# Performance work log

Hardware: AMD Instinct MI355X
Metric: run time of the kernel (lower is better)

The kernel has to match this reference:

```python
import jax, jax.numpy as jnp
import numpy as np

B, T, D = 2, 1024, 1024
NUM_HEADS_ARG = 16
HS = D // NUM_HEADS_ARG          # 64 (per-head size)
H = HS                           # bug in source: num_heads passed = head_size -> 64 heads
FF = 4 * D
EPS = 1e-5


def _layernorm(x, gamma, beta):
    mu = jnp.mean(x, axis=-1, keepdims=True)
    var = jnp.mean(jnp.square(x - mu), axis=-1, keepdims=True)
    return (x - mu) * jax.lax.rsqrt(var + EPS) * gamma + beta


def setup_inputs() -> dict:
    key = jax.random.key(0)
    ks = jax.random.split(key, 12)
    s_d = 1.0 / np.sqrt(D)
    s_cat = 1.0 / np.sqrt(H * HS)
    s_ff = 1.0 / np.sqrt(FF)
    return {
        "x": jax.random.normal(ks[0], (B, T, D), jnp.float32),
        "Wq": jax.random.uniform(ks[1], (H, D, HS), jnp.float32, -s_d, s_d),
        "Wk": jax.random.uniform(ks[2], (H, D, HS), jnp.float32, -s_d, s_d),
        "Wv": jax.random.uniform(ks[3], (H, D, HS), jnp.float32, -s_d, s_d),
        "Wo": jax.random.uniform(ks[4], (H * HS, D), jnp.float32, -s_cat, s_cat),
        "bo": jax.random.uniform(ks[5], (D,), jnp.float32, -s_cat, s_cat),
        "W1": jax.random.uniform(ks[6], (D, FF), jnp.float32, -s_d, s_d),
        "b1": jax.random.uniform(ks[7], (FF,), jnp.float32, -s_d, s_d),
        "W2": jax.random.uniform(ks[8], (FF, D), jnp.float32, -s_ff, s_ff),
        "b2": jax.random.uniform(ks[9], (D,), jnp.float32, -s_ff, s_ff),
        "g1": jnp.ones((D,), jnp.float32),
        "be1": jnp.zeros((D,), jnp.float32),
        "g2": jnp.ones((D,), jnp.float32),
        "be2": jnp.zeros((D,), jnp.float32),
    }


def reference(x, Wq, Wk, Wv, Wo, bo, W1, b1, W2, b2, g1, be1, g2, be2):
    # per-head projections (no bias): [B,H,T,hs]
    q = jnp.einsum('btd,hde->bhte', x, Wq)
    k = jnp.einsum('btd,hde->bhte', x, Wk)
    v = jnp.einsum('btd,hde->bhte', x, Wv)
    scores = jnp.einsum('bhte,bhse->bhts', q, k) / np.sqrt(HS)  # [B,H,T,T]
    causal = jnp.tril(jnp.ones((T, T), bool))
    scores = jnp.where(causal, scores, -jnp.inf)
    probs = jax.nn.softmax(scores, axis=-1)
    att = jnp.einsum('bhts,bhse->bhte', probs, v)               # [B,H,T,hs]
    # torch stack(dim=3) -> [B,T,hs,H] then flatten: index = d*H + h
    cat = jnp.transpose(att, (0, 2, 3, 1)).reshape(B, T, HS * H)
    mha = cat @ Wo + bo
    x1 = _layernorm(x + mha, g1, be1)
    ff = jax.nn.relu(x1 @ W1 + b1) @ W2 + b2
    return _layernorm(x1 + ff, g2, be2)
```

## Files before the change

kernel.cpp:

```cpp
#include <hip/hip_runtime.h>

typedef unsigned short u16;
typedef __bf16 bf16x8 __attribute__((ext_vector_type(8)));
typedef float f32x4 __attribute__((ext_vector_type(4)));

#define B_ 2
#define T_ 1024
#define D_ 1024
#define H_ 64
#define HS_ 64
#define FF_ 4096
#define SZ_QKV 8388608L
#define S_SCALE 0.1803368801111f

__device__ __forceinline__ float bf2f(u16 u) {
  union { unsigned int v; float f; } x; x.v = ((unsigned int)u) << 16; return x.f;
}
__device__ __forceinline__ u16 f2bf(float f) {
  union { float f; unsigned int v; } x; x.f = f;
  unsigned int r = x.v + 0x7fffu + ((x.v >> 16) & 1u);
  return (u16)(r >> 16);
}
__device__ __forceinline__ u16 f2bf_rtz(float f) {
  union { float f; unsigned int v; } x; x.f = f;
  return (u16)(x.v >> 16);
}

typedef __attribute__((address_space(3))) unsigned int lds_u32;
typedef __attribute__((address_space(1))) const unsigned int glb_u32;
__device__ __forceinline__ void gload_lds16(const void* g, void* l) {
  __builtin_amdgcn_global_load_lds((glb_u32*)g, (lds_u32*)l, 16, 0, 0);
}

__global__ __launch_bounds__(256) void prep(
    const float* __restrict__ x, const float* __restrict__ Wq,
    const float* __restrict__ Wk, const float* __restrict__ Wv,
    const float* __restrict__ Wo, const float* __restrict__ W1,
    const float* __restrict__ W2,
    u16* __restrict__ xb, u16* __restrict__ Wqkvt, u16* __restrict__ Wot,
    u16* __restrict__ W1t, u16* __restrict__ W2t)
{
  __shared__ float tile[64][65];
  int id = blockIdx.x;
  if (id < 1024) {
    const long i = ((long)id * 256 + threadIdx.x) * 8;
    float4 a = *(const float4*)(x + i);
    float4 b = *(const float4*)(x + i + 4);
    union { uint4 v; u16 u[8]; } o;
    o.u[0]=f2bf(a.x); o.u[1]=f2bf(a.y); o.u[2]=f2bf(a.z); o.u[3]=f2bf(a.w);
    o.u[4]=f2bf(b.x); o.u[5]=f2bf(b.y); o.u[6]=f2bf(b.z); o.u[7]=f2bf(b.w);
    *(uint4*)(xb + i) = o.v;
    return;
  }
  id -= 1024;
  const float* in; u16* out; long ibase, obase; int in_rs, out_rs, r0, c0;
  if (id < 3072) {
    const int w = id >> 10, rem = id & 1023;
    const int z = rem >> 4, rt = rem & 15;
    in = (w == 0) ? Wq : (w == 1) ? Wk : Wv;
    ibase = (long)z * 65536; in_rs = 64; r0 = rt * 64; c0 = 0;
    out = Wqkvt + (long)w * 4194304;
    obase = (long)z * 65536; out_rs = 1024;
  } else if (id < 4096) {
    const int rem = id - 3072;
    const int z = rem >> 4, ct = rem & 15;
    in = Wo; ibase = (long)z * 1024; in_rs = 65536; r0 = 0; c0 = ct * 64;
    out = Wot; obase = (long)z * 64; out_rs = 4096;
  } else if (id < 5120) {
    const int rem = id - 4096;
    const int rt = rem >> 6, ct = rem & 63;
    in = W1; ibase = 0; in_rs = 4096; r0 = rt * 64; c0 = ct * 64;
    out = W1t; obase = 0; out_rs = 1024;
  } else {
    const int rem = id - 5120;
    const int rt = rem >> 4, ct = rem & 15;
    in = W2; ibase = 0; in_rs = 1024; r0 = rt * 64; c0 = ct * 64;
    out = W2t; obase = 0; out_rs = 4096;
  }
  const int t = threadIdx.x, lr = t >> 4, lc4 = (t & 15) * 4;
  #pragma unroll
  for (int j = 0; j < 4; ++j) {
    float4 f = *(const float4*)(in + ibase + (long)(r0 + lr + j * 16) * in_rs + c0 + lc4);
    tile[lr + j * 16][lc4]     = f.x;
    tile[lr + j * 16][lc4 + 1] = f.y;
    tile[lr + j * 16][lc4 + 2] = f.z;
    tile[lr + j * 16][lc4 + 3] = f.w;
  }
  __syncthreads();
  const int cr = t >> 3, ch = t & 7;
  #pragma unroll
  for (int j2 = 0; j2 < 2; ++j2) {
    const int crr = cr + j2 * 32;
    union { uint4 v; u16 u[8]; } o;
    #pragma unroll
    for (int i = 0; i < 8; ++i) o.u[i] = f2bf(tile[ch * 8 + i][crr]);
    *(uint4*)(out + obase + (long)(c0 + crr) * out_rs + r0 + ch * 8) = o.v;
  }
}

template<int EPI, int LDA, int LDB>
__global__ __launch_bounds__(512, 2) void gemm8b(
    const u16* __restrict__ A, const u16* __restrict__ Bt, u16* __restrict__ C,
    const float* __restrict__ bias, int K, int koff, int ldc)
{
  __shared__ __attribute__((aligned(16))) u16 As[3][256 * 64];
  __shared__ __attribute__((aligned(16))) u16 Bs[3][128 * 64];
  const int nwg = gridDim.x, cpx = nwg >> 3;
  const int sid = (blockIdx.x & 7) * cpx + (blockIdx.x >> 3);
  const int bm = sid & 7, bn = sid >> 3;
  const int bz = blockIdx.z;
  const long ko = (long)bz * koff;
  const int tid = threadIdx.x, wave = tid >> 6, lane = tid & 63;
  const int quad = lane >> 4, l16 = lane & 15;
  const int wm = (wave >> 1) * 64;
  const int wn = (wave & 1) * 64;
  const int slog = ((tid & 7) ^ ((tid >> 3) & 7)) * 8;
  const int srow = tid >> 3;
  const int ph0 = ((quad)     ^ (l16 & 7)) * 8;
  const int ph1 = ((4 + quad) ^ (l16 & 7)) * 8;

  const u16* Ag = A + (long)(bm * 256) * LDA + ko + slog;
  const u16* Bg = Bt + (long)(bn * 128) * LDB + ko + slog;

  f32x4 acc[4][4];
  #pragma unroll
  for (int i = 0; i < 4; ++i)
    #pragma unroll
    for (int j = 0; j < 4; ++j) acc[i][j] = (f32x4){0.f, 0.f, 0.f, 0.f};

  const int nK = K >> 6;

  auto STAGE_A = [&](int d, int t, int a) {
    gload_lds16(Ag + (long)(a * 64 + srow) * LDA + (t << 6),
                (u16*)As[d] + a * 4096 + tid * 8);
  };
  auto STAGE_B = [&](int d, int t, int b) {
    gload_lds16(Bg + (long)(b * 64 + srow) * LDB + (t << 6),
                (u16*)Bs[d] + b * 4096 + tid * 8);
  };

  #pragma unroll
  for (int a = 0; a < 4; ++a) STAGE_A(0, 0, a);
  STAGE_B(0, 0, 0); STAGE_B(0, 0, 1);
  #pragma unroll
  for (int a = 0; a < 4; ++a) STAGE_A(1, 1, a);
  STAGE_B(1, 1, 0); STAGE_B(1, 1, 1);

  bf16x8 af[4][2], bf[4][2];
  int cur = 0;
  for (int t = 0; t < nK; ++t) {
    const int nxt = (cur >= 1) ? cur - 1 : 2;
    const bool st = (t + 2) < nK;
    const u16* Ab = As[cur];
    const u16* Bb = Bs[cur];

    if (t < nK - 1) { asm volatile("s_waitcnt vmcnt(6)" ::: "memory"); }
    else            { asm volatile("s_waitcnt vmcnt(0)" ::: "memory"); }
    __builtin_amdgcn_sched_barrier(0);
    __builtin_amdgcn_s_barrier();
    __builtin_amdgcn_sched_barrier(0);

    #pragma unroll
    for (int ii = 0; ii < 2; ++ii) {
      const u16* r = Ab + (wm + ii * 16 + l16) * 64;
      af[ii][0] = *(const bf16x8*)(r + ph0);
      af[ii][1] = *(const bf16x8*)(r + ph1);
    }
    #pragma unroll
    for (int jj = 0; jj < 2; ++jj) {
      const u16* r = Bb + (wn + jj * 16 + l16) * 64;
      bf[jj][0] = *(const bf16x8*)(r + ph0);
      bf[jj][1] = *(const bf16x8*)(r + ph1);
    }
    #pragma unroll
    for (int jj = 0; jj < 2; ++jj) {
      const u16* r = Bb + (wn + (2 + jj) * 16 + l16) * 64;
      bf[2 + jj][0] = *(const bf16x8*)(r + ph0);
      bf[2 + jj][1] = *(const bf16x8*)(r + ph1);
    }
    #pragma unroll
    for (int ii = 0; ii < 2; ++ii) {
      const u16* r = Ab + (wm + (2 + ii) * 16 + l16) * 64;
      af[2 + ii][0] = *(const bf16x8*)(r + ph0);
      af[2 + ii][1] = *(const bf16x8*)(r + ph1);
    }

    if (st) { STAGE_A(nxt, t + 2, 0); STAGE_A(nxt, t + 2, 1); }
    __builtin_amdgcn_s_setprio(1);
    #pragma unroll
    for (int ks = 0; ks < 2; ++ks)
      #pragma unroll
      for (int ii = 0; ii < 2; ++ii)
        #pragma unroll
        for (int jj = 0; jj < 2; ++jj)
          acc[ii][jj] = __builtin_amdgcn_mfma_f32_16x16x32_bf16(af[ii][ks], bf[jj][ks], acc[ii][jj], 0, 0, 0);
    __builtin_amdgcn_s_setprio(0);

    if (st) { STAGE_A(nxt, t + 2, 2); STAGE_A(nxt, t + 2, 3); }
    __builtin_amdgcn_s_setprio(1);
    #pragma unroll
    for (int ks = 0; ks < 2; ++ks)
      #pragma unroll
      for (int ii = 0; ii < 2; ++ii)
        #pragma unroll
        for (int jj = 0; jj < 2; ++jj)
          acc[ii][2 + jj] = __builtin_amdgcn_mfma_f32_16x16x32_bf16(af[ii][ks], bf[2 + jj][ks], acc[ii][2 + jj], 0, 0, 0);
    __builtin_amdgcn_s_setprio(0);

    if (st) { STAGE_B(nxt, t + 2, 0); STAGE_B(nxt, t + 2, 1); }
    __builtin_amdgcn_s_setprio(1);
    #pragma unroll
    for (int ks = 0; ks < 2; ++ks)
      #pragma unroll
      for (int ii = 0; ii < 2; ++ii)
        #pragma unroll
        for (int jj = 0; jj < 2; ++jj)
          acc[2 + ii][jj] = __builtin_amdgcn_mfma_f32_16x16x32_bf16(af[2 + ii][ks], bf[jj][ks], acc[2 + ii][jj], 0, 0, 0);
    __builtin_amdgcn_s_setprio(0);

    __builtin_amdgcn_s_setprio(1);
    #pragma unroll
    for (int ks = 0; ks < 2; ++ks)
      #pragma unroll
      for (int ii = 0; ii < 2; ++ii)
        #pragma unroll
        for (int jj = 0; jj < 2; ++jj)
          acc[2 + ii][2 + jj] = __builtin_amdgcn_mfma_f32_16x16x32_bf16(af[2 + ii][ks], bf[2 + jj][ks], acc[2 + ii][2 + jj], 0, 0, 0);
    __builtin_amdgcn_s_setprio(0);
    __builtin_amdgcn_sched_barrier(0);

    cur = (cur == 2) ? 0 : cur + 1;
  }

  float bv[4];
  #pragma unroll
  for (int j = 0; j < 4; ++j)
    bv[j] = (EPI == 1) ? bias[bn * 128 + wn + j * 16 + l16] : 0.f;
  #pragma unroll
  for (int i = 0; i < 4; ++i) {
    #pragma unroll
    for (int r = 0; r < 4; ++r) {
      const int row = bm * 256 + wm + i * 16 + quad * 4 + r;
      #pragma unroll
      for (int j = 0; j < 4; ++j) {
        const int col = bn * 128 + wn + j * 16 + l16;
        float vv = acc[i][j][r] + bv[j];
        if (EPI == 1) vv = fmaxf(vv, 0.f);
        if (EPI == 2) {
          const int which = col >> 12, rem = col & 4095;
          const int h = rem >> 6, e = rem & 63;
          const int bb = row >> 10, tt = row & 1023;
          C[(long)which * SZ_QKV + ((long)((bb << 6) + h)) * 65536L + tt * 64 + e] = f2bf(vv);
        } else if (EPI == 3) {
          ((float*)C)[(long)bz * 2097152 + (long)row * ldc + col] = vv;
        } else {
          C[(long)row * ldc + col] = f2bf(vv);
        }
      }
    }
  }
}

__global__ __launch_bounds__(256) void attn_flash(
    const u16* __restrict__ Q, const u16* __restrict__ Kg,
    const u16* __restrict__ V, u16* __restrict__ Om)
{
  __shared__ __attribute__((aligned(16))) u16 Ks[2][64][72];
  __shared__ __attribute__((aligned(16))) u16 Vs[2][64][72];
  __shared__ __attribute__((aligned(16))) u16 QP[4][16][72];
  const int bh = blockIdx.x;
  const int qt = gridDim.y - 1 - blockIdx.y;
  const int b = bh >> 6, h = bh & 63;
  const long base = (long)bh * (T_ * HS_);
  const int tid = threadIdx.x;
  const int wave = tid >> 6, lane = tid & 63, quad = lane >> 4, l16 = lane & 15;
  const int sm = tid >> 2, sc = (tid & 3) * 16;
  const int vswz = (sc >> 4) << 3;

  {
    const int qr = lane >> 3, qe = (lane & 7) * 8;
    #pragma unroll
    for (int j = 0; j < 2; ++j) {
      union { uint4 v; u16 u[8]; } a, o;
      a.v = *(const uint4*)(Q + base + (long)(qt * 64 + wave * 16 + qr + j * 8) * HS_ + qe);
      #pragma unroll
      for (int i = 0; i < 8; ++i) o.u[i] = f2bf(bf2f(a.u[i]) * S_SCALE);
      *(uint4*)&QP[wave][qr + j * 8][qe] = o.v;
    }
  }
  bf16x8 aq0 = *(const bf16x8*)&QP[wave][l16][quad * 8];
  bf16x8 aq1 = *(const bf16x8*)&QP[wave][l16][32 + quad * 8];

  float psum[4] = { 0.f, 0.f, 0.f, 0.f };
  f32x4 oacc[4] = { {0,0,0,0}, {0,0,0,0}, {0,0,0,0}, {0,0,0,0} };

  uint4 kA, kB, vA, vB;
  kA = *(const uint4*)(Kg + base + (long)sm * HS_ + sc);
  kB = *(const uint4*)(Kg + base + (long)sm * HS_ + sc + 8);
  vA = *(const uint4*)(V  + base + (long)sm * HS_ + sc);
  vB = *(const uint4*)(V  + base + (long)sm * HS_ + sc + 8);
  {
    *(uint4*)&Ks[0][sm][sc] = kA; *(uint4*)&Ks[0][sm][sc + 8] = kB;
    union { uint4 v; u16 u[8]; } t0, t1; t0.v = vA; t1.v = vB;
    #pragma unroll
    for (int i = 0; i < 8; ++i) Vs[0][sc + i][sm ^ vswz] = t0.u[i];
    #pragma unroll
    for (int i = 0; i < 8; ++i) Vs[0][sc + 8 + i][sm ^ vswz] = t1.u[i];
  }
  __syncthreads();

  for (int kt = 0; kt <= qt; ++kt) {
    const int cur = kt & 1;
    const bool pf = (kt < qt);
    if (pf) {
      const long nb = base + (long)((kt + 1) * 64 + sm) * HS_ + sc;
      kA = *(const uint4*)(Kg + nb); kB = *(const uint4*)(Kg + nb + 8);
      vA = *(const uint4*)(V  + nb); vB = *(const uint4*)(V  + nb + 8);
    }

    f32x4 sacc[4] = { {0,0,0,0}, {0,0,0,0}, {0,0,0,0}, {0,0,0,0} };
    #pragma unroll
    for (int nt = 0; nt < 4; ++nt) {
      bf16x8 b0 = *(const bf16x8*)&Ks[cur][nt * 16 + l16][quad * 8];
      bf16x8 b1 = *(const bf16x8*)&Ks[cur][nt * 16 + l16][32 + quad * 8];
      sacc[nt] = __builtin_amdgcn_mfma_f32_16x16x32_bf16(aq0, b0, sacc[nt], 0, 0, 0);
      sacc[nt] = __builtin_amdgcn_mfma_f32_16x16x32_bf16(aq1, b1, sacc[nt], 0, 0, 0);
    }

    if (kt == qt) {
      #pragma unroll
      for (int nt = 0; nt < 4; ++nt) {
        const int col = nt * 16 + l16;
        #pragma unroll
        for (int r = 0; r < 4; ++r) {
          const int row = wave * 16 + quad * 4 + r;
          float p = exp2f(sacc[nt][r]);
          p = (col <= row) ? p : 0.f;
          sacc[nt][r] = p; psum[r] += p;
        }
      }
    } else {
      #pragma unroll
      for (int nt = 0; nt < 4; ++nt)
        #pragma unroll
        for (int r = 0; r < 4; ++r) {
          const float p = exp2f(sacc[nt][r]);
          sacc[nt][r] = p; psum[r] += p;
        }
    }

    #pragma unroll
    for (int nt = 0; nt < 4; ++nt)
      #pragma unroll
      for (int r = 0; r < 4; ++r)
        QP[wave][quad * 4 + r][nt * 16 + l16] = f2bf_rtz(sacc[nt][r]);
    bf16x8 p0 = *(const bf16x8*)&QP[wave][l16][quad * 8];
    bf16x8 p1 = *(const bf16x8*)&QP[wave][l16][32 + quad * 8];

    #pragma unroll
    for (int et = 0; et < 4; ++et) {
      const int c0 = ((quad ^ et) * 8);
      bf16x8 b0 = *(const bf16x8*)&Vs[cur][et * 16 + l16][c0];
      bf16x8 b1 = *(const bf16x8*)&Vs[cur][et * 16 + l16][32 + c0];
      oacc[et] = __builtin_amdgcn_mfma_f32_16x16x32_bf16(p0, b0, oacc[et], 0, 0, 0);
      oacc[et] = __builtin_amdgcn_mfma_f32_16x16x32_bf16(p1, b1, oacc[et], 0, 0, 0);
    }

    if (pf) {
      const int nxt = 1 - cur;
      *(uint4*)&Ks[nxt][sm][sc] = kA; *(uint4*)&Ks[nxt][sm][sc + 8] = kB;
      union { uint4 v; u16 u[8]; } t0, t1; t0.v = vA; t1.v = vB;
      #pragma unroll
      for (int i = 0; i < 8; ++i) Vs[nxt][sc + i][sm ^ vswz] = t0.u[i];
      #pragma unroll
      for (int i = 0; i < 8; ++i) Vs[nxt][sc + 8 + i][sm ^ vswz] = t1.u[i];
    }
    __syncthreads();
  }

  #pragma unroll
  for (int off = 1; off < 16; off <<= 1)
    #pragma unroll
    for (int r = 0; r < 4; ++r)
      psum[r] += __shfl_xor(psum[r], off, 64);
  u16 (*Os)[72] = Ks[0];
  #pragma unroll
  for (int r = 0; r < 4; ++r) {
    const float rinv = 1.f / fmaxf(psum[r], 1e-20f);
    const int row = wave * 16 + quad * 4 + r;
    #pragma unroll
    for (int et = 0; et < 4; ++et)
      Os[row][et * 16 + l16] = f2bf(oacc[et][r] * rinv);
  }
  const int orow = wave * 16 + (lane >> 3), oe = (lane & 7) * 8;
  #pragma unroll
  for (int it = 0; it < 2; ++it) {
    const int rr = orow + it * 8;
    uint4 o = *(const uint4*)&Os[rr][oe];
    *(uint4*)(Om + ((long)(b * T_ + qt * 64 + rr)) * 4096 + h * 64 + oe) = o;
  }
}

template<int XBF, int OBF>
__global__ __launch_bounds__(256) void ln_sum4(
    const float* __restrict__ P4, const float* __restrict__ bias,
    const void* __restrict__ Xv, const float* __restrict__ g,
    const float* __restrict__ be, void* __restrict__ outv)
{
  __shared__ float red[8];
  const int row = blockIdx.x, tid = threadIdx.x;
  const long base = (long)row * D_;
  float v4[4]; float s = 0.f;
  #pragma unroll
  for (int j = 0; j < 4; ++j) {
    const int i = tid + j * 256;
    float acc = bias[i];
    #pragma unroll
    for (int p = 0; p < 4; ++p) acc += P4[(long)p * 2097152 + base + i];
    const float xval = XBF ? bf2f(((const u16*)Xv)[base + i]) : ((const float*)Xv)[base + i];
    v4[j] = xval + acc;
    s += v4[j];
  }
  #pragma unroll
  for (int off = 32; off > 0; off >>= 1) s += __shfl_down(s, off, 64);
  if ((tid & 63) == 0) red[tid >> 6] = s;
  __syncthreads();
  const float mu = (red[0] + red[1] + red[2] + red[3]) * (1.f / D_);
  float vs = 0.f;
  #pragma unroll
  for (int j = 0; j < 4; ++j) { const float d = v4[j] - mu; vs += d * d; }
  #pragma unroll
  for (int off = 32; off > 0; off >>= 1) vs += __shfl_down(vs, off, 64);
  __syncthreads();
  if ((tid & 63) == 0) red[tid >> 6] = vs;
  __syncthreads();
  const float rs = rsqrtf((red[0] + red[1] + red[2] + red[3]) * (1.f / D_) + 1e-5f);
  #pragma unroll
  for (int j = 0; j < 4; ++j) {
    const int i = tid + j * 256;
    const float o = (v4[j] - mu) * rs * g[i] + be[i];
    if (OBF) ((u16*)outv)[base + i] = f2bf(o);
    else     ((float*)outv)[base + i] = o;
  }
}

extern "C" void kernel_launch(void* const* d_in, const int* in_sizes, int n_in,
                              void* d_out, int out_size, void* d_ws, size_t ws_size,
                              hipStream_t stream) {
  const float* x   = (const float*)d_in[0];
  const float* Wq  = (const float*)d_in[1];
  const float* Wk  = (const float*)d_in[2];
  const float* Wv  = (const float*)d_in[3];
  const float* Wo  = (const float*)d_in[4];
  const float* bo  = (const float*)d_in[5];
  const float* W1  = (const float*)d_in[6];
  const float* b1  = (const float*)d_in[7];
  const float* W2  = (const float*)d_in[8];
  const float* b2  = (const float*)d_in[9];
  const float* g1  = (const float*)d_in[10];
  const float* be1 = (const float*)d_in[11];
  const float* g2  = (const float*)d_in[12];
  const float* be2 = (const float*)d_in[13];
  float* out = (float*)d_out;

  u16* ws = (u16*)d_ws;
  u16* xb    = ws;
  u16* Wqkvt = xb + 2097152;
  u16* Wot   = Wqkvt + 12582912;
  u16* W1t   = Wot + 4194304;
  u16* W2t   = W1t + 4194304;
  u16* q     = W2t + 4194304;
  u16* k     = q + SZ_QKV;
  u16* v     = k + SZ_QKV;
  u16* Om    = v + SZ_QKV;
  float* P1 = (float*)q;
  float* P2 = (float*)q;
  u16* x1  = v;
  u16* h1  = Om;

  dim3 blk(256);
  dim3 blk8(512);

  prep<<<dim3(7168), blk, 0, stream>>>(x, Wq, Wk, Wv, Wo, W1, W2,
                                       xb, Wqkvt, Wot, W1t, W2t);

  gemm8b<2, 1024, 1024><<<dim3(768), blk8, 0, stream>>>(
      xb, Wqkvt, q, nullptr, 1024, 0, 0);

  attn_flash<<<dim3(128, 16), blk, 0, stream>>>(q, k, v, Om);

  gemm8b<3, 4096, 4096><<<dim3(64, 1, 4), blk8, 0, stream>>>(
      Om, Wot, (u16*)P1, nullptr, 1024, 1024, 1024);

  ln_sum4<0, 1><<<dim3(2048), blk, 0, stream>>>(P1, bo, x, g1, be1, x1);

  gemm8b<1, 1024, 1024><<<dim3(256), blk8, 0, stream>>>(
      x1, W1t, h1, b1, 1024, 0, 4096);

  gemm8b<3, 4096, 4096><<<dim3(64, 1, 4), blk8, 0, stream>>>(
      h1, W2t, (u16*)P2, nullptr, 1024, 1024, 1024);

  ln_sum4<1, 0><<<dim3(2048), blk, 0, stream>>>(P2, b2, x1, g2, be2, out);

  (void)in_sizes; (void)n_in; (void)out_size; (void)ws_size;
}
```

Measured before the change: 357.8 us.

## Write V transposed from QKV GEMM and vectorize layernorm loads

The QKV projection epilogue now stores V in a transposed [e][t] layout per head. The attention kernel can therefore copy V tiles into shared memory with 16-byte stores, replacing the scalar transposing scatter with XOR swizzle. Separately, the layernorm-sum kernel now uses float4 and ushort4 vector loads and stores, with each thread handling four contiguous elements. The V epilogue writes become strided along t, which may hurt coalescing in the GEMM store path, and dropping the swizzle may bring back LDS bank conflicts on the V reads.

After: 381.0 us. +6.5%, slower.

```diff
diff --git a/kernel.cpp b/kernel.cpp
--- a/kernel.cpp
+++ b/kernel.cpp
@@ -250,7 +250,12 @@
           const int which = col >> 12, rem = col & 4095;
           const int h = rem >> 6, e = rem & 63;
           const int bb = row >> 10, tt = row & 1023;
-          C[(long)which * SZ_QKV + ((long)((bb << 6) + h)) * 65536L + tt * 64 + e] = f2bf(vv);
+          long off;
+          if (which == 2)
+            off = 2L * SZ_QKV + ((long)((bb << 6) + h)) * 65536L + (long)e * 1024 + tt;
+          else
+            off = (long)which * SZ_QKV + ((long)((bb << 6) + h)) * 65536L + (long)tt * 64 + e;
+          C[off] = f2bf(vv);
         } else if (EPI == 3) {
           ((float*)C)[(long)bz * 2097152 + (long)row * ldc + col] = vv;
         } else {
@@ -263,7 +268,7 @@
 
 __global__ __launch_bounds__(256) void attn_flash(
     const u16* __restrict__ Q, const u16* __restrict__ Kg,
-    const u16* __restrict__ V, u16* __restrict__ Om)
+    const u16* __restrict__ Vt, u16* __restrict__ Om)
 {
   __shared__ __attribute__((aligned(16))) u16 Ks[2][64][72];
   __shared__ __attribute__((aligned(16))) u16 Vs[2][64][72];
@@ -275,7 +280,6 @@
   const int tid = threadIdx.x;
   const int wave = tid >> 6, lane = tid & 63, quad = lane >> 4, l16 = lane & 15;
   const int sm = tid >> 2, sc = (tid & 3) * 16;
-  const int vswz = (sc >> 4) << 3;
 
   {
     const int qr = lane >> 3, qe = (lane & 7) * 8;
@@ -297,15 +301,11 @@
   uint4 kA, kB, vA, vB;
   kA = *(const uint4*)(Kg + base + (long)sm * HS_ + sc);
   kB = *(const uint4*)(Kg + base + (long)sm * HS_ + sc + 8);
-  vA = *(const uint4*)(V  + base + (long)sm * HS_ + sc);
-  vB = *(const uint4*)(V  + base + (long)sm * HS_ + sc + 8);
+  vA = *(const uint4*)(Vt + base + (long)sm * 1024 + sc);
+  vB = *(const uint4*)(Vt + base + (long)sm * 1024 + sc + 8);
   {
     *(uint4*)&Ks[0][sm][sc] = kA; *(uint4*)&Ks[0][sm][sc + 8] = kB;
-    union { uint4 v; u16 u[8]; } t0, t1; t0.v = vA; t1.v = vB;
-    #pragma unroll
-    for (int i = 0; i < 8; ++i) Vs[0][sc + i][sm ^ vswz] = t0.u[i];
-    #pragma unroll
-    for (int i = 0; i < 8; ++i) Vs[0][sc + 8 + i][sm ^ vswz] = t1.u[i];
+    *(uint4*)&Vs[0][sm][sc] = vA; *(uint4*)&Vs[0][sm][sc + 8] = vB;
   }
   __syncthreads();
 
@@ -313,9 +313,10 @@
     const int cur = kt & 1;
     const bool pf = (kt < qt);
     if (pf) {
-      const long nb = base + (long)((kt + 1) * 64 + sm) * HS_ + sc;
-      kA = *(const uint4*)(Kg + nb); kB = *(const uint4*)(Kg + nb + 8);
-      vA = *(const uint4*)(V  + nb); vB = *(const uint4*)(V  + nb + 8);
+      kA = *(const uint4*)(Kg + base + (long)((kt + 1) * 64 + sm) * HS_ + sc);
+      kB = *(const uint4*)(Kg + base + (long)((kt + 1) * 64 + sm) * HS_ + sc + 8);
+      vA = *(const uint4*)(Vt + base + (long)sm * 1024 + (kt + 1) * 64 + sc);
+      vB = *(const uint4*)(Vt + base + (long)sm * 1024 + (kt + 1) * 64 + sc + 8);
     }
 
     f32x4 sacc[4] = { {0,0,0,0}, {0,0,0,0}, {0,0,0,0}, {0,0,0,0} };
@@ -359,9 +360,8 @@
 
     #pragma unroll
     for (int et = 0; et < 4; ++et) {
-      const int c0 = ((quad ^ et) * 8);
-      bf16x8 b0 = *(const bf16x8*)&Vs[cur][et * 16 + l16][c0];
-      bf16x8 b1 = *(const bf16x8*)&Vs[cur][et * 16 + l16][32 + c0];
+      bf16x8 b0 = *(const bf16x8*)&Vs[cur][et * 16 + l16][quad * 8];
+      bf16x8 b1 = *(const bf16x8*)&Vs[cur][et * 16 + l16][32 + quad * 8];
       oacc[et] = __builtin_amdgcn_mfma_f32_16x16x32_bf16(p0, b0, oacc[et], 0, 0, 0);
       oacc[et] = __builtin_amdgcn_mfma_f32_16x16x32_bf16(p1, b1, oacc[et], 0, 0, 0);
     }
@@ -369,11 +369,7 @@
     if (pf) {
       const int nxt = 1 - cur;
       *(uint4*)&Ks[nxt][sm][sc] = kA; *(uint4*)&Ks[nxt][sm][sc + 8] = kB;
-      union { uint4 v; u16 u[8]; } t0, t1; t0.v = vA; t1.v = vB;
-      #pragma unroll
-      for (int i = 0; i < 8; ++i) Vs[nxt][sc + i][sm ^ vswz] = t0.u[i];
-      #pragma unroll
-      for (int i = 0; i < 8; ++i) Vs[nxt][sc + 8 + i][sm ^ vswz] = t1.u[i];
+      *(uint4*)&Vs[nxt][sm][sc] = vA; *(uint4*)&Vs[nxt][sm][sc + 8] = vB;
     }
     __syncthreads();
   }
@@ -410,17 +406,25 @@
   __shared__ float red[8];
   const int row = blockIdx.x, tid = threadIdx.x;
   const long base = (long)row * D_;
-  float v4[4]; float s = 0.f;
-  #pragma unroll
-  for (int j = 0; j < 4; ++j) {
-    const int i = tid + j * 256;
-    float acc = bias[i];
-    #pragma unroll
-    for (int p = 0; p < 4; ++p) acc += P4[(long)p * 2097152 + base + i];
-    const float xval = XBF ? bf2f(((const u16*)Xv)[base + i]) : ((const float*)Xv)[base + i];
-    v4[j] = xval + acc;
-    s += v4[j];
-  }
+  const int i0 = tid * 4;
+
+  float4 a = *(const float4*)(bias + i0);
+  #pragma unroll
+  for (int p = 0; p < 4; ++p) {
+    float4 pv = *(const float4*)(P4 + (long)p * 2097152 + base + i0);
+    a.x += pv.x; a.y += pv.y; a.z += pv.z; a.w += pv.w;
+  }
+  float v4[4];
+  if (XBF) {
+    ushort4 xu = *(const ushort4*)((const u16*)Xv + base + i0);
+    v4[0] = bf2f(xu.x) + a.x; v4[1] = bf2f(xu.y) + a.y;
+    v4[2] = bf2f(xu.z) + a.z; v4[3] = bf2f(xu.w) + a.w;
+  } else {
+    float4 xv = *(const float4*)((const float*)Xv + base + i0);
+    v4[0] = xv.x + a.x; v4[1] = xv.y + a.y;
+    v4[2] = xv.z + a.z; v4[3] = xv.w + a.w;
+  }
+  float s = v4[0] + v4[1] + v4[2] + v4[3];
   #pragma unroll
   for (int off = 32; off > 0; off >>= 1) s += __shfl_down(s, off, 64);
   if ((tid & 63) == 0) red[tid >> 6] = s;
@@ -435,12 +439,18 @@
   if ((tid & 63) == 0) red[tid >> 6] = vs;
   __syncthreads();
   const float rs = rsqrtf((red[0] + red[1] + red[2] + red[3]) * (1.f / D_) + 1e-5f);
-  #pragma unroll
-  for (int j = 0; j < 4; ++j) {
-    const int i = tid + j * 256;
-    const float o = (v4[j] - mu) * rs * g[i] + be[i];
-    if (OBF) ((u16*)outv)[base + i] = f2bf(o);
-    else     ((float*)outv)[base + i] = o;
+  const float4 gv = *(const float4*)(g + i0);
+  const float4 bev = *(const float4*)(be + i0);
+  const float o0 = (v4[0] - mu) * rs * gv.x + bev.x;
+  const float o1 = (v4[1] - mu) * rs * gv.y + bev.y;
+  const float o2 = (v4[2] - mu) * rs * gv.z + bev.z;
+  const float o3 = (v4[3] - mu) * rs * gv.w + bev.w;
+  if (OBF) {
+    ushort4 ou = { f2bf(o0), f2bf(o1), f2bf(o2), f2bf(o3) };
+    *(ushort4*)((u16*)outv + base + i0) = ou;
+  } else {
+    float4 of = { o0, o1, o2, o3 };
+    *(float4*)((float*)outv + base + i0) = of;
   }
 }
 
```
